# Optimization experiments

Hardware: AMD Instinct MI355X
Metric: run time of the kernel (lower is better)

Reference implementation:

```python
import jax, jax.numpy as jnp
import numpy as np

B, IN_CH, SLOTS, SLOT_SIZE, READ_SLOTS = 16, 512, 10000, 256, 3


def _fa_params(key, c, scale=0.02):
    k1, k2 = jax.random.split(key)
    return (jax.random.normal(k1, (c, c), jnp.float32) * scale, jnp.zeros((c,), jnp.float32),
            jax.random.normal(k2, (c, c), jnp.float32) * scale, jnp.zeros((c,), jnp.float32))


def fast_attention(x, w1, b1, w2, b2):
    # FastAttention: x * Linear2(softmax(Linear1(x), dim=channel))
    h = jax.nn.softmax(x @ w1 + b1, axis=1)
    return x * (h @ w2 + b2)


def setup_inputs() -> dict:
    key = jax.random.key(0)
    ks = jax.random.split(key, 12)
    s = 0.02
    inp = {}
    inp["inputs"] = jax.random.normal(ks[0], (B, IN_CH), jnp.float32)
    inp["memory"] = jax.random.normal(ks[1], (B, SLOTS, SLOT_SIZE), jnp.float32)
    # read_weights branch: FastAttention(IN_CH) -> Linear(IN_CH, READ_SLOTS*SLOTS) -> tanh
    inp["fa_r_w1"], inp["fa_r_b1"], inp["fa_r_w2"], inp["fa_r_b2"] = _fa_params(ks[2], IN_CH)
    inp["W_read"] = jax.random.normal(ks[3], (IN_CH, READ_SLOTS * SLOTS), jnp.float32) * s
    inp["b_read"] = jnp.zeros((READ_SLOTS * SLOTS,), jnp.float32)
    # update_weights branch: FastAttention(IN_CH) -> Linear(IN_CH, READ_SLOTS) -> sigmoid
    inp["fa_u_w1"], inp["fa_u_b1"], inp["fa_u_w2"], inp["fa_u_b2"] = _fa_params(ks[4], IN_CH)
    inp["W_uw"] = jax.random.normal(ks[5], (IN_CH, READ_SLOTS), jnp.float32) * s
    inp["b_uw"] = jnp.zeros((READ_SLOTS,), jnp.float32)
    # update_memory branch: FastAttention(IN_CH+SLOT_SIZE) -> Linear(., SLOT_SIZE) -> relu
    inp["fa_um_w1"], inp["fa_um_b1"], inp["fa_um_w2"], inp["fa_um_b2"] = _fa_params(ks[6], IN_CH + SLOT_SIZE)
    inp["W_um"] = jax.random.normal(ks[7], (IN_CH + SLOT_SIZE, SLOT_SIZE), jnp.float32) * s
    inp["b_um"] = jnp.zeros((SLOT_SIZE,), jnp.float32)
    # apply_memory branch: FastAttention(2*SLOT_SIZE) -> Linear(., SLOT_SIZE) -> relu
    inp["fa_am_w1"], inp["fa_am_b1"], inp["fa_am_w2"], inp["fa_am_b2"] = _fa_params(ks[8], 2 * SLOT_SIZE)
    inp["W_am"] = jax.random.normal(ks[9], (2 * SLOT_SIZE, SLOT_SIZE), jnp.float32) * s
    inp["b_am"] = jnp.zeros((SLOT_SIZE,), jnp.float32)
    return inp


def reference(inputs, memory,
              fa_r_w1, fa_r_b1, fa_r_w2, fa_r_b2, W_read, b_read,
              fa_u_w1, fa_u_b1, fa_u_w2, fa_u_b2, W_uw, b_uw,
              fa_um_w1, fa_um_b1, fa_um_w2, fa_um_b2, W_um, b_um,
              fa_am_w1, fa_am_b1, fa_am_w2, fa_am_b2, W_am, b_am):
    b = inputs.shape[0]
    # read scores: [B, READ_SLOTS, SLOTS]
    read = jnp.tanh(fast_attention(inputs, fa_r_w1, fa_r_b1, fa_r_w2, fa_r_b2) @ W_read + b_read)
    read = read.reshape(b, READ_SLOTS, SLOTS)
    read_w = jnp.max(read, axis=2)                 # [B, READ_SLOTS]
    read_idx = jnp.argmax(read, axis=2)            # [B, READ_SLOTS] int
    upd_w = jax.nn.sigmoid(fast_attention(inputs, fa_u_w1, fa_u_b1, fa_u_w2, fa_u_b2) @ W_uw + b_uw)
    # gather the selected memory slots: [B, READ_SLOTS, SLOT_SIZE]
    r_all = memory[jnp.arange(b)[:, None], read_idx]
    m = jnp.zeros((b, SLOT_SIZE), inputs.dtype)
    # sequential recurrence over the (small, fixed) read_slots
    for i in range(READ_SLOTS):
        r = r_all[:, i]                            # [B, SLOT_SIZE]
        upd = jax.nn.relu(fast_attention(jnp.concatenate([r, inputs], axis=1),
                                         fa_um_w1, fa_um_b1, fa_um_w2, fa_um_b2) @ W_um + b_um)
        u = upd_w[:, i:i + 1]
        r = u * upd + (1.0 - u) * r
        m = read_w[:, i:i + 1] * jax.nn.relu(fast_attention(jnp.concatenate([r, m], axis=1),
                                                            fa_am_w1, fa_am_b1, fa_am_w2, fa_am_b2) @ W_am + b_am)
    return jnp.tanh(m)
```

## Files before the change

### kernel.cpp

```cpp
#include <hip/hip_runtime.h>
#include <cfloat>
#include <cmath>

constexpr int NTILES = 79;

enum : int {
  WS_XR    = 0,
  WS_UPDW  = 8192,
  WS_READW = 8240,
  WS_PMAX  = 8288,
  WS_PIDX  = 12080,
  WS_RNEW  = 15872,
  WS_M     = 28160,
  WS_XC    = 32256,
  WS_TPA   = 69120,
  WS_HA    = 134656,
  WS_YPA   = 151040,
  WS_TPU   = 216576,
  WS_HU    = 437760,
  WS_YPU   = 474624,
  WS_WPU   = 695808,
  WS_TPM   = 769536,
  WS_HM    = 802304,
  WS_YPM   = 810496,
  WS_WPM   = 843264,
};

__device__ __forceinline__ float wave_sum(float v) {
#pragma unroll
  for (int o = 32; o > 0; o >>= 1) v += __shfl_xor(v, o);
  return v;
}
__device__ __forceinline__ float wave_max(float v) {
#pragma unroll
  for (int o = 32; o > 0; o >>= 1) v = fmaxf(v, __shfl_xor(v, o));
  return v;
}
__device__ __forceinline__ float block_sum(float v, float* red) {
  int lane = threadIdx.x & 63, w = threadIdx.x >> 6, nw = blockDim.x >> 6;
  v = wave_sum(v);
  __syncthreads();
  if (lane == 0) red[w] = v;
  __syncthreads();
  float s = 0.f;
  for (int k = 0; k < nw; k++) s += red[k];
  return s;
}
__device__ __forceinline__ float block_max(float v, float* red) {
  int lane = threadIdx.x & 63, w = threadIdx.x >> 6, nw = blockDim.x >> 6;
  v = wave_max(v);
  __syncthreads();
  if (lane == 0) red[w] = v;
  __syncthreads();
  float s = -FLT_MAX;
  for (int k = 0; k < nw; k++) s = fmaxf(s, red[k]);
  return s;
}

__device__ __forceinline__ void mm_tile16(
    const float* __restrict__ xs,
    const float* __restrict__ W, int ldw,
    int koff, int jbase, float2& ra, float2& rb) {
  int lane = threadIdx.x & 63, w = threadIdx.x >> 6;
  const float* xa = xs + (w * 2) * 128;
  const float* xb = xa + 128;
  const float* Wp = W + (size_t)koff * ldw + jbase + lane * 2;
  float a00 = 0.f, a01 = 0.f, a10 = 0.f, a11 = 0.f;
#pragma unroll 8
  for (int k = 0; k < 128; k++) {
    float2 wv = *(const float2*)(Wp + (size_t)k * ldw);
    float xav = xa[k], xbv = xb[k];
    a00 = fmaf(xav, wv.x, a00); a01 = fmaf(xav, wv.y, a01);
    a10 = fmaf(xbv, wv.x, a10); a11 = fmaf(xbv, wv.y, a11);
  }
  ra = make_float2(a00, a01);
  rb = make_float2(a10, a11);
}
__device__ __forceinline__ void store_tile16(
    float* __restrict__ T, int ldt, int jbase, float2 ra, float2 rb) {
  int lane = threadIdx.x & 63, w = threadIdx.x >> 6;
  int r0 = w * 2, j0 = jbase + lane * 2;
  *(float2*)(T + (size_t)r0 * ldt + j0) = ra;
  *(float2*)(T + (size_t)(r0 + 1) * ldt + j0) = rb;
}

__global__ __launch_bounds__(512) void k_mm1_a(
    const float* __restrict__ x, const float* __restrict__ w1r,
    const float* __restrict__ w1u, float* __restrict__ TPA) {
  __shared__ float xs[16 * 128];
  int jt = blockIdx.x, ks = blockIdx.y, m = blockIdx.z, tid = threadIdx.x;
  for (int t = tid; t < 2048; t += 512) {
    int b = t >> 7, kk = t & 127;
    xs[t] = x[b * 512 + ks * 128 + kk];
  }
  __syncthreads();
  float2 ra, rb;
  mm_tile16(xs, m ? w1u : w1r, 512, ks * 128, jt * 128, ra, rb);
  store_tile16(TPA + (size_t)((m * 4 + ks) * 16) * 512, 512, jt * 128, ra, rb);
}

__global__ __launch_bounds__(512) void k_sm_a(
    const float* __restrict__ TPA, const float* __restrict__ b1r,
    const float* __restrict__ b1u, float* __restrict__ HA) {
  __shared__ float red[16];
  int b = blockIdx.x, m = blockIdx.y, tid = threadIdx.x;
  float t = (m ? b1u : b1r)[tid];
#pragma unroll
  for (int ks = 0; ks < 4; ks++)
    t += TPA[(size_t)((m * 4 + ks) * 16 + b) * 512 + tid];
  float mx = block_max(t, red);
  float e = expf(t - mx);
  float s = block_sum(e, red);
  HA[(size_t)(m * 16 + b) * 512 + tid] = e / s;
}

__global__ __launch_bounds__(512) void k_mm2_a(
    const float* __restrict__ HA, const float* __restrict__ w2r,
    const float* __restrict__ w2u, float* __restrict__ YPA) {
  __shared__ float xs[16 * 128];
  int jt = blockIdx.x, ks = blockIdx.y, m = blockIdx.z, tid = threadIdx.x;
  for (int t = tid; t < 2048; t += 512) {
    int b = t >> 7, kk = t & 127;
    xs[t] = HA[(size_t)(m * 16 + b) * 512 + ks * 128 + kk];
  }
  __syncthreads();
  float2 ra, rb;
  mm_tile16(xs, m ? w2u : w2r, 512, ks * 128, jt * 128, ra, rb);
  store_tile16(YPA + (size_t)((m * 4 + ks) * 16) * 512, 512, jt * 128, ra, rb);
}

__global__ __launch_bounds__(512) void k_fin_a(
    const float* __restrict__ x, const float* __restrict__ YPA,
    const float* __restrict__ b2r, const float* __restrict__ b2u,
    const float* __restrict__ Wuw, const float* __restrict__ buw,
    float* __restrict__ XR, float* __restrict__ UPDW, float* __restrict__ M) {
  __shared__ float red[16];
  int b = blockIdx.x, tid = threadIdx.x;
  float yr = b2r[tid], yu = b2u[tid];
#pragma unroll
  for (int ks = 0; ks < 4; ks++) {
    yr += YPA[(size_t)((0 + ks) * 16 + b) * 512 + tid];
    yu += YPA[(size_t)((4 + ks) * 16 + b) * 512 + tid];
  }
  float xv = x[b * 512 + tid];
  XR[b * 512 + tid] = xv * yr;
  float xu = xv * yu;
  if (tid < 256) M[b * 256 + tid] = 0.f;
  for (int i = 0; i < 3; i++) {
    float si = block_sum(xu * Wuw[tid * 3 + i], red);
    if (tid == 0) UPDW[b * 3 + i] = 1.f / (1.f + expf(-(si + buw[i])));
  }
}

__global__ __launch_bounds__(512) void k_read(
    const float* __restrict__ W, const float* __restrict__ brd,
    const float* __restrict__ xr,
    float* __restrict__ pmax, int* __restrict__ pidx) {
  __shared__ __align__(16) float xs[16 * 512];
  int tid = threadIdx.x, lane = tid & 63, w = tid >> 6;
  int i = blockIdx.y, tile = blockIdx.x;
  {
    const float4* s4 = (const float4*)xr;
    float4* d4 = (float4*)xs;
    for (int t = tid; t < 2048; t += 512) d4[t] = s4[t];
  }
  __syncthreads();
  int b0 = w * 2, b1 = b0 + 1;
  int s0 = tile * 128 + lane * 2;
  int sC = (s0 > 9998) ? 9998 : s0;
  const float* Wp = W + i * 10000 + sC;
  const float* xap = xs + b0 * 512;
  const float* xbp = xs + b1 * 512;
  float a00 = 0.f, a01 = 0.f, a10 = 0.f, a11 = 0.f;
#pragma unroll 8
  for (int c = 0; c < 512; c += 4) {
    float4 xa = *(const float4*)(xap + c);
    float4 xb = *(const float4*)(xbp + c);
    float2 w0 = *(const float2*)(Wp + (size_t)(c + 0) * 30000);
    float2 w1 = *(const float2*)(Wp + (size_t)(c + 1) * 30000);
    float2 w2 = *(const float2*)(Wp + (size_t)(c + 2) * 30000);
    float2 w3 = *(const float2*)(Wp + (size_t)(c + 3) * 30000);
    a00 = fmaf(xa.x, w0.x, a00); a01 = fmaf(xa.x, w0.y, a01);
    a10 = fmaf(xb.x, w0.x, a10); a11 = fmaf(xb.x, w0.y, a11);
    a00 = fmaf(xa.y, w1.x, a00); a01 = fmaf(xa.y, w1.y, a01);
    a10 = fmaf(xb.y, w1.x, a10); a11 = fmaf(xb.y, w1.y, a11);
    a00 = fmaf(xa.z, w2.x, a00); a01 = fmaf(xa.z, w2.y, a01);
    a10 = fmaf(xb.z, w2.x, a10); a11 = fmaf(xb.z, w2.y, a11);
    a00 = fmaf(xa.w, w3.x, a00); a01 = fmaf(xa.w, w3.y, a01);
    a10 = fmaf(xb.w, w3.x, a10); a11 = fmaf(xb.w, w3.y, a11);
  }
  float2 bb = *(const float2*)(brd + i * 10000 + sC);
  bool ok0 = (s0 < 10000), ok1 = (s0 + 1 < 10000);
  float v00 = a00 + bb.x, v01 = a01 + bb.y;
  float v10 = a10 + bb.x, v11 = a11 + bb.y;
  float bv0 = ok0 ? v00 : -FLT_MAX; int bi0 = s0;
  if (ok1 && v01 > bv0) { bv0 = v01; bi0 = s0 + 1; }
  float bv1 = ok0 ? v10 : -FLT_MAX; int bi1 = s0;
  if (ok1 && v11 > bv1) { bv1 = v11; bi1 = s0 + 1; }
#pragma unroll
  for (int o = 32; o > 0; o >>= 1) {
    float ov = __shfl_down(bv0, o); int oi = __shfl_down(bi0, o);
    if (ov > bv0) { bv0 = ov; bi0 = oi; }
    ov = __shfl_down(bv1, o); oi = __shfl_down(bi1, o);
    if (ov > bv1) { bv1 = ov; bi1 = oi; }
  }
  if (lane == 0) {
    int base = (i * 16 + b0) * NTILES + tile;
    pmax[base] = bv0; pidx[base] = bi0;
    base = (i * 16 + b1) * NTILES + tile;
    pmax[base] = bv1; pidx[base] = bi1;
  }
}

__global__ __launch_bounds__(768) void k_gather(
    const float* __restrict__ mem, const float* __restrict__ x,
    const float* __restrict__ pmax, const int* __restrict__ pidx,
    float* __restrict__ READW, float* __restrict__ XC) {
  __shared__ int sidx;
  int bi = blockIdx.x, b = bi / 3, i = bi % 3;
  int tid = threadIdx.x, lane = tid & 63;
  if (tid < 64) {
    float bv = -FLT_MAX; int bix = 0;
    const float* pm = pmax + (i * 16 + b) * NTILES;
    const int* pi = pidx + (i * 16 + b) * NTILES;
    for (int t = lane; t < NTILES; t += 64) {
      float v = pm[t]; int ix = pi[t];
      if (v > bv || (v == bv && ix < bix)) { bv = v; bix = ix; }
    }
#pragma unroll
    for (int o = 32; o > 0; o >>= 1) {
      float ov = __shfl_down(bv, o); int oi = __shfl_down(bix, o);
      if (ov > bv || (ov == bv && oi < bix)) { bv = ov; bix = oi; }
    }
    if (lane == 0) { sidx = bix; READW[bi] = tanhf(bv); }
  }
  __syncthreads();
  if (tid < 256) XC[(size_t)bi * 768 + tid] = mem[((size_t)b * 10000 + sidx) * 256 + tid];
  else           XC[(size_t)bi * 768 + tid] = x[b * 512 + (tid - 256)];
}

__global__ __launch_bounds__(512) void k_mm1_u(
    const float* __restrict__ XC, const float* __restrict__ w1um,
    float* __restrict__ TPU) {
  __shared__ float xs[16 * 128];
  int jt = blockIdx.x, ks = blockIdx.y, g = blockIdx.z, tid = threadIdx.x;
  for (int t = tid; t < 2048; t += 512) {
    int r = t >> 7, kk = t & 127;
    xs[t] = XC[(size_t)(g * 16 + r) * 768 + ks * 128 + kk];
  }
  __syncthreads();
  float2 ra, rb;
  mm_tile16(xs, w1um, 768, ks * 128, jt * 128, ra, rb);
  store_tile16(TPU + (size_t)(ks * 48 + g * 16) * 768, 768, jt * 128, ra, rb);
}

__global__ __launch_bounds__(768) void k_sm_u(
    const float* __restrict__ TPU, const float* __restrict__ b1um,
    float* __restrict__ HU) {
  __shared__ float red[16];
  int bi = blockIdx.x, tid = threadIdx.x;
  float t = b1um[tid];
#pragma unroll
  for (int ks = 0; ks < 6; ks++)
    t += TPU[(size_t)(ks * 48 + bi) * 768 + tid];
  float mx = block_max(t, red);
  float e = expf(t - mx);
  float s = block_sum(e, red);
  HU[(size_t)bi * 768 + tid] = e / s;
}

__global__ __launch_bounds__(512) void k_mm2_u(
    const float* __restrict__ HU, const float* __restrict__ w2um,
    float* __restrict__ YPU) {
  __shared__ float xs[16 * 128];
  int jt = blockIdx.x, ks = blockIdx.y, g = blockIdx.z, tid = threadIdx.x;
  for (int t = tid; t < 2048; t += 512) {
    int r = t >> 7, kk = t & 127;
    xs[t] = HU[(size_t)(g * 16 + r) * 768 + ks * 128 + kk];
  }
  __syncthreads();
  float2 ra, rb;
  mm_tile16(xs, w2um, 768, ks * 128, jt * 128, ra, rb);
  store_tile16(YPU + (size_t)(ks * 48 + g * 16) * 768, 768, jt * 128, ra, rb);
}

__global__ __launch_bounds__(512) void k_wum(
    const float* __restrict__ YPU, const float* __restrict__ XC,
    const float* __restrict__ b2um, const float* __restrict__ Wum,
    float* __restrict__ WPU) {
  __shared__ float xs[16 * 128];
  int jt = blockIdx.x, ks = blockIdx.y, g = blockIdx.z, tid = threadIdx.x;
  for (int t = tid; t < 2048; t += 512) {
    int r = t >> 7, kk = t & 127;
    int bi = g * 16 + r, k = ks * 128 + kk;
    float y = b2um[k];
#pragma unroll
    for (int k2 = 0; k2 < 6; k2++) y += YPU[(size_t)(k2 * 48 + bi) * 768 + k];
    xs[t] = XC[(size_t)bi * 768 + k] * y;
  }
  __syncthreads();
  float2 ra, rb;
  mm_tile16(xs, Wum, 256, ks * 128, jt * 128, ra, rb);
  store_tile16(WPU + (size_t)(ks * 48 + g * 16) * 256, 256, jt * 128, ra, rb);
}

__global__ __launch_bounds__(256) void k_fin_u(
    const float* __restrict__ WPU, const float* __restrict__ XC,
    const float* __restrict__ bum, const float* __restrict__ UPDW,
    float* __restrict__ RNEW) {
  int bi = blockIdx.x, tid = threadIdx.x;
  float s = bum[tid];
#pragma unroll
  for (int ks = 0; ks < 6; ks++)
    s += WPU[(size_t)(ks * 48 + bi) * 256 + tid];
  float u = UPDW[bi];
  RNEW[(size_t)bi * 256 + tid] = u * fmaxf(s, 0.f) + (1.f - u) * XC[(size_t)bi * 768 + tid];
}

__global__ __launch_bounds__(512) void k_mm1_m(
    const float* __restrict__ RNEW, const float* __restrict__ M,
    const float* __restrict__ w1am, float* __restrict__ TPM, int i) {
  __shared__ float xs[16 * 128];
  int jt = blockIdx.x, ks = blockIdx.y, tid = threadIdx.x;
  for (int t = tid; t < 2048; t += 512) {
    int b = t >> 7, kk = t & 127;
    xs[t] = (ks < 2) ? RNEW[(size_t)(b * 3 + i) * 256 + ks * 128 + kk]
                     : M[b * 256 + (ks - 2) * 128 + kk];
  }
  __syncthreads();
  float2 ra, rb;
  mm_tile16(xs, w1am, 512, ks * 128, jt * 128, ra, rb);
  store_tile16(TPM + (size_t)(ks * 16) * 512, 512, jt * 128, ra, rb);
}

__global__ __launch_bounds__(512) void k_sm_m(
    const float* __restrict__ TPM, const float* __restrict__ b1am,
    float* __restrict__ HM) {
  __shared__ float red[16];
  int b = blockIdx.x, tid = threadIdx.x;
  float t = b1am[tid];
#pragma unroll
  for (int ks = 0; ks < 4; ks++)
    t += TPM[(size_t)(ks * 16 + b) * 512 + tid];
  float mx = block_max(t, red);
  float e = expf(t - mx);
  float s = block_sum(e, red);
  HM[(size_t)b * 512 + tid] = e / s;
}

__global__ __launch_bounds__(512) void k_mm2_m(
    const float* __restrict__ HM, const float* __restrict__ w2am,
    float* __restrict__ YPM) {
  __shared__ float xs[16 * 128];
  int jt = blockIdx.x, ks = blockIdx.y, tid = threadIdx.x;
  for (int t = tid; t < 2048; t += 512) {
    int b = t >> 7, kk = t & 127;
    xs[t] = HM[(size_t)b * 512 + ks * 128 + kk];
  }
  __syncthreads();
  float2 ra, rb;
  mm_tile16(xs, w2am, 512, ks * 128, jt * 128, ra, rb);
  store_tile16(YPM + (size_t)(ks * 16) * 512, 512, jt * 128, ra, rb);
}

__global__ __launch_bounds__(512) void k_wam(
    const float* __restrict__ YPM, const float* __restrict__ RNEW,
    const float* __restrict__ M, const float* __restrict__ b2am,
    const float* __restrict__ Wam, float* __restrict__ WPM, int i) {
  __shared__ float xs[16 * 128];
  int jt = blockIdx.x, ks = blockIdx.y, tid = threadIdx.x;
  for (int t = tid; t < 2048; t += 512) {
    int b = t >> 7, kk = t & 127;
    int k = ks * 128 + kk;
    float xc = (ks < 2) ? RNEW[(size_t)(b * 3 + i) * 256 + k]
                        : M[b * 256 + k - 256];
    float y = b2am[k];
#pragma unroll
    for (int k2 = 0; k2 < 4; k2++) y += YPM[(size_t)(k2 * 16 + b) * 512 + k];
    xs[t] = xc * y;
  }
  __syncthreads();
  float2 ra, rb;
  mm_tile16(xs, Wam, 256, ks * 128, jt * 128, ra, rb);
  store_tile16(WPM + (size_t)(ks * 16) * 256, 256, jt * 128, ra, rb);
}

__global__ __launch_bounds__(256) void k_fin_m(
    const float* __restrict__ WPM, const float* __restrict__ bam,
    const float* __restrict__ READW, float* __restrict__ M,
    float* __restrict__ out, int i, int last) {
  int b = blockIdx.x, tid = threadIdx.x;
  float s = bam[tid];
#pragma unroll
  for (int ks = 0; ks < 4; ks++)
    s += WPM[(size_t)(ks * 16 + b) * 256 + tid];
  float mv = READW[b * 3 + i] * fmaxf(s, 0.f);
  M[b * 256 + tid] = mv;
  if (last) out[b * 256 + tid] = tanhf(mv);
}

extern "C" void kernel_launch(void* const* d_in, const int* in_sizes, int n_in,
                              void* d_out, int out_size, void* d_ws, size_t ws_size,
                              hipStream_t stream) {
  const float* x    = (const float*)d_in[0];
  const float* mem  = (const float*)d_in[1];
  const float* w1r  = (const float*)d_in[2];
  const float* b1r  = (const float*)d_in[3];
  const float* w2r  = (const float*)d_in[4];
  const float* b2r  = (const float*)d_in[5];
  const float* Wrd  = (const float*)d_in[6];
  const float* brd  = (const float*)d_in[7];
  const float* w1u  = (const float*)d_in[8];
  const float* b1u  = (const float*)d_in[9];
  const float* w2u  = (const float*)d_in[10];
  const float* b2u  = (const float*)d_in[11];
  const float* Wuw  = (const float*)d_in[12];
  const float* buw  = (const float*)d_in[13];
  const float* w1um = (const float*)d_in[14];
  const float* b1um = (const float*)d_in[15];
  const float* w2um = (const float*)d_in[16];
  const float* b2um = (const float*)d_in[17];
  const float* Wum  = (const float*)d_in[18];
  const float* bum  = (const float*)d_in[19];
  const float* w1am = (const float*)d_in[20];
  const float* b1am = (const float*)d_in[21];
  const float* w2am = (const float*)d_in[22];
  const float* b2am = (const float*)d_in[23];
  const float* Wam  = (const float*)d_in[24];
  const float* bam  = (const float*)d_in[25];

  float* ws   = (float*)d_ws;
  float* XR   = ws + WS_XR;
  float* UPDW = ws + WS_UPDW;
  float* RDW  = ws + WS_READW;
  float* PMAX = ws + WS_PMAX;
  int*   PIDX = (int*)(ws + WS_PIDX);
  float* RNEW = ws + WS_RNEW;
  float* M    = ws + WS_M;
  float* XC   = ws + WS_XC;
  float* TPA  = ws + WS_TPA;
  float* HA   = ws + WS_HA;
  float* YPA  = ws + WS_YPA;
  float* TPU  = ws + WS_TPU;
  float* HU   = ws + WS_HU;
  float* YPU  = ws + WS_YPU;
  float* WPU  = ws + WS_WPU;
  float* TPM  = ws + WS_TPM;
  float* HM   = ws + WS_HM;
  float* YPM  = ws + WS_YPM;
  float* WPM  = ws + WS_WPM;
  float* out  = (float*)d_out;

  k_mm1_a<<<dim3(4, 4, 2), 512, 0, stream>>>(x, w1r, w1u, TPA);
  k_sm_a <<<dim3(16, 2),   512, 0, stream>>>(TPA, b1r, b1u, HA);
  k_mm2_a<<<dim3(4, 4, 2), 512, 0, stream>>>(HA, w2r, w2u, YPA);
  k_fin_a<<<16,            512, 0, stream>>>(x, YPA, b2r, b2u, Wuw, buw,
                                             XR, UPDW, M);
  k_read  <<<dim3(NTILES, 3), 512, 0, stream>>>(Wrd, brd, XR, PMAX, PIDX);
  k_gather<<<48,              768, 0, stream>>>(mem, x, PMAX, PIDX, RDW, XC);
  k_mm1_u<<<dim3(6, 6, 3), 512, 0, stream>>>(XC, w1um, TPU);
  k_sm_u <<<48,            768, 0, stream>>>(TPU, b1um, HU);
  k_mm2_u<<<dim3(6, 6, 3), 512, 0, stream>>>(HU, w2um, YPU);
  k_wum  <<<dim3(2, 6, 3), 512, 0, stream>>>(YPU, XC, b2um, Wum, WPU);
  k_fin_u<<<48,            256, 0, stream>>>(WPU, XC, bum, UPDW, RNEW);
  for (int i = 0; i < 3; i++) {
    k_mm1_m<<<dim3(4, 4), 512, 0, stream>>>(RNEW, M, w1am, TPM, i);
    k_sm_m <<<16,         512, 0, stream>>>(TPM, b1am, HM);
    k_mm2_m<<<dim3(4, 4), 512, 0, stream>>>(HM, w2am, YPM);
    k_wam  <<<dim3(2, 4), 512, 0, stream>>>(YPM, RNEW, M, b2am, Wam, WPM, i);
    k_fin_m<<<16,         256, 0, stream>>>(WPM, bam, RDW, M, out, i, i == 2);
  }
}
```

Measured before the change: 508.1 us.

## Fuse all stages into one cooperative persistent kernel with grid barriers

Replaces the chain of about 26 small kernel launches with a single cooperative kernel of 256 blocks that steps through the stages, separated by atomic grid-wide barriers. It also fuses softmax with the second FastAttention matmul and the x-multiply, so the HA/YPA/HU/YPU intermediate buffers go away. The aim is to remove per-launch overhead and the tiny-grid tail latency that dominate this latency-bound chain. In exchange, stages with few blocks leave most CUs idle, each block now does more serial work (the full K=512/768 reduction), and every barrier costs a global atomic spin.

```diff
diff --git a/kernel.cpp b/kernel.cpp
--- a/kernel.cpp
+++ b/kernel.cpp
@@ -14,16 +14,23 @@
   WS_M     = 28160,
   WS_XC    = 32256,
   WS_TPA   = 69120,
-  WS_HA    = 134656,
-  WS_YPA   = 151040,
+  WS_BAR   = 134656,
+  WS_XU    = 151040,
   WS_TPU   = 216576,
-  WS_HU    = 437760,
-  WS_YPU   = 474624,
-  WS_WPU   = 695808,
+  WS_XU2   = 474624,
   WS_TPM   = 769536,
-  WS_HM    = 802304,
-  WS_YPM   = 810496,
-  WS_WPM   = 843264,
+  WS_XA    = 810496,
+};
+
+struct Params {
+  const float *x, *mem;
+  const float *w1r, *b1r, *w2r, *b2r, *Wrd, *brd;
+  const float *w1u, *b1u, *w2u, *b2u, *Wuw, *buw;
+  const float *w1um, *b1um, *w2um, *b2um, *Wum, *bum;
+  const float *w1am, *b1am, *w2am, *b2am, *Wam, *bam;
+  float *XR, *XU, *UPDW, *RDW, *PMAX;
+  int   *PIDX;
+  float *RNEW, *M, *XC, *TPA, *TPU, *XU2, *TPM, *XA, *out;
 };
 
 __device__ __forceinline__ float wave_sum(float v) {
@@ -46,28 +53,28 @@
   for (int k = 0; k < nw; k++) s += red[k];
   return s;
 }
-__device__ __forceinline__ float block_max(float v, float* red) {
-  int lane = threadIdx.x & 63, w = threadIdx.x >> 6, nw = blockDim.x >> 6;
-  v = wave_max(v);
+
+__device__ __forceinline__ void grid_sync(unsigned* bar, unsigned target) {
   __syncthreads();
-  if (lane == 0) red[w] = v;
+  if (threadIdx.x == 0) {
+    __threadfence();
+    __hip_atomic_fetch_add(bar, 1u, __ATOMIC_RELEASE, __HIP_MEMORY_SCOPE_AGENT);
+    while (__hip_atomic_load(bar, __ATOMIC_ACQUIRE, __HIP_MEMORY_SCOPE_AGENT) < target)
+      __builtin_amdgcn_s_sleep(2);
+  }
   __syncthreads();
-  float s = -FLT_MAX;
-  for (int k = 0; k < nw; k++) s = fmaxf(s, red[k]);
-  return s;
-}
-
-__device__ __forceinline__ void mm_tile16(
-    const float* __restrict__ xs,
-    const float* __restrict__ W, int ldw,
-    int koff, int jbase, float2& ra, float2& rb) {
+}
+
+__device__ __forceinline__ void mm_rows(const float* __restrict__ xs, int ldx, int K,
+                                        const float* __restrict__ W, int ldw, int jbase,
+                                        float2& ra, float2& rb) {
   int lane = threadIdx.x & 63, w = threadIdx.x >> 6;
-  const float* xa = xs + (w * 2) * 128;
-  const float* xb = xa + 128;
-  const float* Wp = W + (size_t)koff * ldw + jbase + lane * 2;
+  const float* xa = xs + (w * 2) * ldx;
+  const float* xb = xa + ldx;
+  const float* Wp = W + jbase + lane * 2;
   float a00 = 0.f, a01 = 0.f, a10 = 0.f, a11 = 0.f;
 #pragma unroll 8
-  for (int k = 0; k < 128; k++) {
+  for (int k = 0; k < K; k++) {
     float2 wv = *(const float2*)(Wp + (size_t)k * ldw);
     float xav = xa[k], xbv = xb[k];
     a00 = fmaf(xav, wv.x, a00); a01 = fmaf(xav, wv.y, a01);
@@ -76,398 +83,347 @@
   ra = make_float2(a00, a01);
   rb = make_float2(a10, a11);
 }
-__device__ __forceinline__ void store_tile16(
-    float* __restrict__ T, int ldt, int jbase, float2 ra, float2 rb) {
+__device__ __forceinline__ void store_tile16(float* __restrict__ T, int ldt, int jbase,
+                                             float2 ra, float2 rb) {
   int lane = threadIdx.x & 63, w = threadIdx.x >> 6;
   int r0 = w * 2, j0 = jbase + lane * 2;
   *(float2*)(T + (size_t)r0 * ldt + j0) = ra;
   *(float2*)(T + (size_t)(r0 + 1) * ldt + j0) = rb;
 }
 
-__global__ __launch_bounds__(512) void k_mm1_a(
-    const float* __restrict__ x, const float* __restrict__ w1r,
-    const float* __restrict__ w1u, float* __restrict__ TPA) {
-  __shared__ float xs[16 * 128];
-  int jt = blockIdx.x, ks = blockIdx.y, m = blockIdx.z, tid = threadIdx.x;
-  for (int t = tid; t < 2048; t += 512) {
-    int b = t >> 7, kk = t & 127;
-    xs[t] = x[b * 512 + ks * 128 + kk];
-  }
-  __syncthreads();
-  float2 ra, rb;
-  mm_tile16(xs, m ? w1u : w1r, 512, ks * 128, jt * 128, ra, rb);
-  store_tile16(TPA + (size_t)((m * 4 + ks) * 16) * 512, 512, jt * 128, ra, rb);
-}
-
-__global__ __launch_bounds__(512) void k_sm_a(
-    const float* __restrict__ TPA, const float* __restrict__ b1r,
-    const float* __restrict__ b1u, float* __restrict__ HA) {
+__device__ __forceinline__ void softmax_rows(float* xs, int ncol) {
+  int lane = threadIdx.x & 63, w = threadIdx.x >> 6;
+#pragma unroll
+  for (int rr = 0; rr < 2; rr++) {
+    float* row = xs + (size_t)(w * 2 + rr) * ncol;
+    float mx = -FLT_MAX;
+    for (int j = lane; j < ncol; j += 64) mx = fmaxf(mx, row[j]);
+    mx = wave_max(mx);
+    float acc = 0.f;
+    for (int j = lane; j < ncol; j += 64) {
+      float e = expf(row[j] - mx);
+      row[j] = e;
+      acc += e;
+    }
+    acc = wave_sum(acc);
+    float inv = 1.f / acc;
+    for (int j = lane; j < ncol; j += 64) row[j] *= inv;
+  }
+}
+
+__global__ __launch_bounds__(512, 2) void mega(Params p, unsigned* bar) {
+  __shared__ __align__(16) float xs[12288];
   __shared__ float red[16];
-  int b = blockIdx.x, m = blockIdx.y, tid = threadIdx.x;
-  float t = (m ? b1u : b1r)[tid];
-#pragma unroll
-  for (int ks = 0; ks < 4; ks++)
-    t += TPA[(size_t)((m * 4 + ks) * 16 + b) * 512 + tid];
-  float mx = block_max(t, red);
-  float e = expf(t - mx);
-  float s = block_sum(e, red);
-  HA[(size_t)(m * 16 + b) * 512 + tid] = e / s;
-}
-
-__global__ __launch_bounds__(512) void k_mm2_a(
-    const float* __restrict__ HA, const float* __restrict__ w2r,
-    const float* __restrict__ w2u, float* __restrict__ YPA) {
-  __shared__ float xs[16 * 128];
-  int jt = blockIdx.x, ks = blockIdx.y, m = blockIdx.z, tid = threadIdx.x;
-  for (int t = tid; t < 2048; t += 512) {
-    int b = t >> 7, kk = t & 127;
-    xs[t] = HA[(size_t)(m * 16 + b) * 512 + ks * 128 + kk];
-  }
-  __syncthreads();
-  float2 ra, rb;
-  mm_tile16(xs, m ? w2u : w2r, 512, ks * 128, jt * 128, ra, rb);
-  store_tile16(YPA + (size_t)((m * 4 + ks) * 16) * 512, 512, jt * 128, ra, rb);
-}
-
-__global__ __launch_bounds__(512) void k_fin_a(
-    const float* __restrict__ x, const float* __restrict__ YPA,
-    const float* __restrict__ b2r, const float* __restrict__ b2u,
-    const float* __restrict__ Wuw, const float* __restrict__ buw,
-    float* __restrict__ XR, float* __restrict__ UPDW, float* __restrict__ M) {
-  __shared__ float red[16];
-  int b = blockIdx.x, tid = threadIdx.x;
-  float yr = b2r[tid], yu = b2u[tid];
-#pragma unroll
-  for (int ks = 0; ks < 4; ks++) {
-    yr += YPA[(size_t)((0 + ks) * 16 + b) * 512 + tid];
-    yu += YPA[(size_t)((4 + ks) * 16 + b) * 512 + tid];
-  }
-  float xv = x[b * 512 + tid];
-  XR[b * 512 + tid] = xv * yr;
-  float xu = xv * yu;
-  if (tid < 256) M[b * 256 + tid] = 0.f;
+  __shared__ int sidx;
+  const int bid = blockIdx.x, tid = threadIdx.x;
+  const int lane = tid & 63, w = tid >> 6;
+  unsigned ph = 0;
+#define GSYNC() do { ++ph; grid_sync(bar, ph * 256u); } while (0)
+
+  if (bid < 32) {
+    int jt = bid & 3, ks = (bid >> 2) & 3, m = bid >> 4;
+    for (int t = tid; t < 2048; t += 512) {
+      int b = t >> 7, kk = t & 127;
+      xs[t] = p.x[b * 512 + ks * 128 + kk];
+    }
+    __syncthreads();
+    float2 ra, rb;
+    mm_rows(xs, 128, 128, (m ? p.w1u : p.w1r) + (size_t)(ks * 128) * 512, 512, jt * 128, ra, rb);
+    store_tile16(p.TPA + (size_t)((m * 4 + ks) * 16) * 512, 512, jt * 128, ra, rb);
+  }
+  GSYNC();
+
+  if (bid < 8) {
+    int m = bid >> 2, jt = bid & 3;
+    const float* b1 = m ? p.b1u : p.b1r;
+    for (int e = tid; e < 8192; e += 512) {
+      int b = e >> 9, j = e & 511;
+      float v = b1[j];
+#pragma unroll
+      for (int ks = 0; ks < 4; ks++) v += p.TPA[(size_t)((m * 4 + ks) * 16 + b) * 512 + j];
+      xs[e] = v;
+    }
+    __syncthreads();
+    softmax_rows(xs, 512);
+    float2 ra, rb;
+    mm_rows(xs, 512, 512, m ? p.w2u : p.w2r, 512, jt * 128, ra, rb);
+    int r0 = w * 2, j0 = jt * 128 + lane * 2;
+    const float* b2 = m ? p.b2u : p.b2r;
+    float b20 = b2[j0], b21 = b2[j0 + 1];
+    float* dst = m ? p.XU : p.XR;
+    float2 x0 = *(const float2*)(p.x + r0 * 512 + j0);
+    float2 x1 = *(const float2*)(p.x + (r0 + 1) * 512 + j0);
+    *(float2*)(dst + r0 * 512 + j0)       = make_float2(x0.x * (ra.x + b20), x0.y * (ra.y + b21));
+    *(float2*)(dst + (r0 + 1) * 512 + j0) = make_float2(x1.x * (rb.x + b20), x1.y * (rb.y + b21));
+  }
+  GSYNC();
+
+  if (bid < 237) {
+    int ii = bid / NTILES, tile = bid % NTILES;
+    {
+      const float4* s4 = (const float4*)p.XR;
+      float4* d4 = (float4*)xs;
+      for (int t = tid; t < 2048; t += 512) d4[t] = s4[t];
+    }
+    __syncthreads();
+    int b0 = w * 2, b1 = b0 + 1;
+    int s0 = tile * 128 + lane * 2;
+    int sC = (s0 > 9998) ? 9998 : s0;
+    const float* Wp = p.Wrd + ii * 10000 + sC;
+    const float* xap = xs + b0 * 512;
+    const float* xbp = xs + b1 * 512;
+    float a00 = 0.f, a01 = 0.f, a10 = 0.f, a11 = 0.f;
+#pragma unroll 8
+    for (int c = 0; c < 512; c += 4) {
+      float4 xa = *(const float4*)(xap + c);
+      float4 xb = *(const float4*)(xbp + c);
+      float2 w0 = *(const float2*)(Wp + (size_t)(c + 0) * 30000);
+      float2 w1 = *(const float2*)(Wp + (size_t)(c + 1) * 30000);
+      float2 w2 = *(const float2*)(Wp + (size_t)(c + 2) * 30000);
+      float2 w3 = *(const float2*)(Wp + (size_t)(c + 3) * 30000);
+      a00 = fmaf(xa.x, w0.x, a00); a01 = fmaf(xa.x, w0.y, a01);
+      a10 = fmaf(xb.x, w0.x, a10); a11 = fmaf(xb.x, w0.y, a11);
+      a00 = fmaf(xa.y, w1.x, a00); a01 = fmaf(xa.y, w1.y, a01);
+      a10 = fmaf(xb.y, w1.x, a10); a11 = fmaf(xb.y, w1.y, a11);
+      a00 = fmaf(xa.z, w2.x, a00); a01 = fmaf(xa.z, w2.y, a01);
+      a10 = fmaf(xb.z, w2.x, a10); a11 = fmaf(xb.z, w2.y, a11);
+      a00 = fmaf(xa.w, w3.x, a00); a01 = fmaf(xa.w, w3.y, a01);
+      a10 = fmaf(xb.w, w3.x, a10); a11 = fmaf(xb.w, w3.y, a11);
+    }
+    float2 bb = *(const float2*)(p.brd + ii * 10000 + sC);
+    bool ok0 = (s0 < 10000), ok1 = (s0 + 1 < 10000);
+    float v00 = a00 + bb.x, v01 = a01 + bb.y;
+    float v10 = a10 + bb.x, v11 = a11 + bb.y;
+    float bv0 = ok0 ? v00 : -FLT_MAX; int bi0 = s0;
+    if (ok1 && v01 > bv0) { bv0 = v01; bi0 = s0 + 1; }
+    float bv1 = ok0 ? v10 : -FLT_MAX; int bi1 = s0;
+    if (ok1 && v11 > bv1) { bv1 = v11; bi1 = s0 + 1; }
+#pragma unroll
+    for (int o = 32; o > 0; o >>= 1) {
+      float ov = __shfl_down(bv0, o); int oi = __shfl_down(bi0, o);
+      if (ov > bv0) { bv0 = ov; bi0 = oi; }
+      ov = __shfl_down(bv1, o); oi = __shfl_down(bi1, o);
+      if (ov > bv1) { bv1 = ov; bi1 = oi; }
+    }
+    if (lane == 0) {
+      int base = (ii * 16 + b0) * NTILES + tile;
+      p.PMAX[base] = bv0; p.PIDX[base] = bi0;
+      base = (ii * 16 + b1) * NTILES + tile;
+      p.PMAX[base] = bv1; p.PIDX[base] = bi1;
+    }
+  } else if (bid >= 240) {
+    int b = bid - 240;
+    float xu = p.XU[b * 512 + tid];
+    if (tid < 256) p.M[b * 256 + tid] = 0.f;
+    for (int i2 = 0; i2 < 3; i2++) {
+      float si = block_sum(xu * p.Wuw[tid * 3 + i2], red);
+      if (tid == 0) p.UPDW[b * 3 + i2] = 1.f / (1.f + expf(-(si + p.buw[i2])));
+    }
+  }
+  GSYNC();
+
+  if (bid < 48) {
+    int b = bid / 3, ii = bid % 3;
+    if (tid < 64) {
+      float bv = -FLT_MAX; int bix = 0;
+      const float* pm = p.PMAX + (ii * 16 + b) * NTILES;
+      const int* pi = p.PIDX + (ii * 16 + b) * NTILES;
+      for (int t = tid; t < NTILES; t += 64) {
+        float v = pm[t]; int ix = pi[t];
+        if (v > bv || (v == bv && ix < bix)) { bv = v; bix = ix; }
+      }
+#pragma unroll
+      for (int o = 32; o > 0; o >>= 1) {
+        float ov = __shfl_down(bv, o); int oi = __shfl_down(bix, o);
+        if (ov > bv || (ov == bv && oi < bix)) { bv = ov; bix = oi; }
+      }
+      if (tid == 0) { sidx = bix; p.RDW[bid] = tanhf(bv); }
+    }
+    __syncthreads();
+    for (int t = tid; t < 768; t += 512)
+      p.XC[(size_t)bid * 768 + t] = (t < 256)
+          ? p.mem[((size_t)b * 10000 + sidx) * 256 + t]
+          : p.x[b * 512 + (t - 256)];
+  }
+  GSYNC();
+
+  if (bid < 108) {
+    int jt = bid % 6, ks = (bid / 6) % 6, g = bid / 36;
+    for (int t = tid; t < 2048; t += 512) {
+      int r = t >> 7, kk = t & 127;
+      xs[t] = p.XC[(size_t)(g * 16 + r) * 768 + ks * 128 + kk];
+    }
+    __syncthreads();
+    float2 ra, rb;
+    mm_rows(xs, 128, 128, p.w1um + (size_t)(ks * 128) * 768, 768, jt * 128, ra, rb);
+    store_tile16(p.TPU + (size_t)(ks * 48 + g * 16) * 768, 768, jt * 128, ra, rb);
+  }
+  GSYNC();
+
+  if (bid < 18) {
+    int g = bid / 6, jt = bid % 6;
+    for (int e = tid; e < 12288; e += 512) {
+      int r = e / 768, j = e - r * 768;
+      float v = p.b1um[j];
+#pragma unroll
+      for (int ks = 0; ks < 6; ks++) v += p.TPU[(size_t)(ks * 48 + g * 16 + r) * 768 + j];
+      xs[e] = v;
+    }
+    __syncthreads();
+    softmax_rows(xs, 768);
+    float2 ra, rb;
+    mm_rows(xs, 768, 768, p.w2um, 768, jt * 128, ra, rb);
+    int r0 = w * 2, j0 = jt * 128 + lane * 2, bi0 = g * 16 + r0;
+    float b0 = p.b2um[j0], b1v = p.b2um[j0 + 1];
+    float2 xc0 = *(const float2*)(p.XC + (size_t)bi0 * 768 + j0);
+    float2 xc1 = *(const float2*)(p.XC + (size_t)(bi0 + 1) * 768 + j0);
+    *(float2*)(p.XU2 + (size_t)bi0 * 768 + j0) =
+        make_float2(xc0.x * (ra.x + b0), xc0.y * (ra.y + b1v));
+    *(float2*)(p.XU2 + (size_t)(bi0 + 1) * 768 + j0) =
+        make_float2(xc1.x * (rb.x + b0), xc1.y * (rb.y + b1v));
+  }
+  GSYNC();
+
+  if (bid < 6) {
+    int g = bid >> 1, jt = bid & 1;
+    const float* src = p.XU2 + (size_t)(g * 16) * 768;
+    for (int e = tid; e < 12288; e += 512) xs[e] = src[e];
+    __syncthreads();
+    float2 ra, rb;
+    mm_rows(xs, 768, 768, p.Wum, 256, jt * 128, ra, rb);
+    int r0 = w * 2, j0 = jt * 128 + lane * 2, bi0 = g * 16 + r0;
+    float bb0 = p.bum[j0], bb1 = p.bum[j0 + 1];
+    float u0 = p.UPDW[bi0], u1 = p.UPDW[bi0 + 1];
+    float2 xc0 = *(const float2*)(p.XC + (size_t)bi0 * 768 + j0);
+    float2 xc1 = *(const float2*)(p.XC + (size_t)(bi0 + 1) * 768 + j0);
+    *(float2*)(p.RNEW + (size_t)bi0 * 256 + j0) =
+        make_float2(u0 * fmaxf(ra.x + bb0, 0.f) + (1.f - u0) * xc0.x,
+                    u0 * fmaxf(ra.y + bb1, 0.f) + (1.f - u0) * xc0.y);
+    *(float2*)(p.RNEW + (size_t)(bi0 + 1) * 256 + j0) =
+        make_float2(u1 * fmaxf(rb.x + bb0, 0.f) + (1.f - u1) * xc1.x,
+                    u1 * fmaxf(rb.y + bb1, 0.f) + (1.f - u1) * xc1.y);
+  }
+  GSYNC();
+
   for (int i = 0; i < 3; i++) {
-    float si = block_sum(xu * Wuw[tid * 3 + i], red);
-    if (tid == 0) UPDW[b * 3 + i] = 1.f / (1.f + expf(-(si + buw[i])));
-  }
-}
-
-__global__ __launch_bounds__(512) void k_read(
-    const float* __restrict__ W, const float* __restrict__ brd,
-    const float* __restrict__ xr,
-    float* __restrict__ pmax, int* __restrict__ pidx) {
-  __shared__ __align__(16) float xs[16 * 512];
-  int tid = threadIdx.x, lane = tid & 63, w = tid >> 6;
-  int i = blockIdx.y, tile = blockIdx.x;
-  {
-    const float4* s4 = (const float4*)xr;
-    float4* d4 = (float4*)xs;
-    for (int t = tid; t < 2048; t += 512) d4[t] = s4[t];
-  }
-  __syncthreads();
-  int b0 = w * 2, b1 = b0 + 1;
-  int s0 = tile * 128 + lane * 2;
-  int sC = (s0 > 9998) ? 9998 : s0;
-  const float* Wp = W + i * 10000 + sC;
-  const float* xap = xs + b0 * 512;
-  const float* xbp = xs + b1 * 512;
-  float a00 = 0.f, a01 = 0.f, a10 = 0.f, a11 = 0.f;
-#pragma unroll 8
-  for (int c = 0; c < 512; c += 4) {
-    float4 xa = *(const float4*)(xap + c);
-    float4 xb = *(const float4*)(xbp + c);
-    float2 w0 = *(const float2*)(Wp + (size_t)(c + 0) * 30000);
-    float2 w1 = *(const float2*)(Wp + (size_t)(c + 1) * 30000);
-    float2 w2 = *(const float2*)(Wp + (size_t)(c + 2) * 30000);
-    float2 w3 = *(const float2*)(Wp + (size_t)(c + 3) * 30000);
-    a00 = fmaf(xa.x, w0.x, a00); a01 = fmaf(xa.x, w0.y, a01);
-    a10 = fmaf(xb.x, w0.x, a10); a11 = fmaf(xb.x, w0.y, a11);
-    a00 = fmaf(xa.y, w1.x, a00); a01 = fmaf(xa.y, w1.y, a01);
-    a10 = fmaf(xb.y, w1.x, a10); a11 = fmaf(xb.y, w1.y, a11);
-    a00 = fmaf(xa.z, w2.x, a00); a01 = fmaf(xa.z, w2.y, a01);
-    a10 = fmaf(xb.z, w2.x, a10); a11 = fmaf(xb.z, w2.y, a11);
-    a00 = fmaf(xa.w, w3.x, a00); a01 = fmaf(xa.w, w3.y, a01);
-    a10 = fmaf(xb.w, w3.x, a10); a11 = fmaf(xb.w, w3.y, a11);
-  }
-  float2 bb = *(const float2*)(brd + i * 10000 + sC);
-  bool ok0 = (s0 < 10000), ok1 = (s0 + 1 < 10000);
-  float v00 = a00 + bb.x, v01 = a01 + bb.y;
-  float v10 = a10 + bb.x, v11 = a11 + bb.y;
-  float bv0 = ok0 ? v00 : -FLT_MAX; int bi0 = s0;
-  if (ok1 && v01 > bv0) { bv0 = v01; bi0 = s0 + 1; }
-  float bv1 = ok0 ? v10 : -FLT_MAX; int bi1 = s0;
-  if (ok1 && v11 > bv1) { bv1 = v11; bi1 = s0 + 1; }
-#pragma unroll
-  for (int o = 32; o > 0; o >>= 1) {
-    float ov = __shfl_down(bv0, o); int oi = __shfl_down(bi0, o);
-    if (ov > bv0) { bv0 = ov; bi0 = oi; }
-    ov = __shfl_down(bv1, o); oi = __shfl_down(bi1, o);
-    if (ov > bv1) { bv1 = ov; bi1 = oi; }
-  }
-  if (lane == 0) {
-    int base = (i * 16 + b0) * NTILES + tile;
-    pmax[base] = bv0; pidx[base] = bi0;
-    base = (i * 16 + b1) * NTILES + tile;
-    pmax[base] = bv1; pidx[base] = bi1;
-  }
-}
-
-__global__ __launch_bounds__(768) void k_gather(
-    const float* __restrict__ mem, const float* __restrict__ x,
-    const float* __restrict__ pmax, const int* __restrict__ pidx,
-    float* __restrict__ READW, float* __restrict__ XC) {
-  __shared__ int sidx;
-  int bi = blockIdx.x, b = bi / 3, i = bi % 3;
-  int tid = threadIdx.x, lane = tid & 63;
-  if (tid < 64) {
-    float bv = -FLT_MAX; int bix = 0;
-    const float* pm = pmax + (i * 16 + b) * NTILES;
-    const int* pi = pidx + (i * 16 + b) * NTILES;
-    for (int t = lane; t < NTILES; t += 64) {
-      float v = pm[t]; int ix = pi[t];
-      if (v > bv || (v == bv && ix < bix)) { bv = v; bix = ix; }
-    }
-#pragma unroll
-    for (int o = 32; o > 0; o >>= 1) {
-      float ov = __shfl_down(bv, o); int oi = __shfl_down(bix, o);
-      if (ov > bv || (ov == bv && oi < bix)) { bv = ov; bix = oi; }
-    }
-    if (lane == 0) { sidx = bix; READW[bi] = tanhf(bv); }
-  }
-  __syncthreads();
-  if (tid < 256) XC[(size_t)bi * 768 + tid] = mem[((size_t)b * 10000 + sidx) * 256 + tid];
-  else           XC[(size_t)bi * 768 + tid] = x[b * 512 + (tid - 256)];
-}
-
-__global__ __launch_bounds__(512) void k_mm1_u(
-    const float* __restrict__ XC, const float* __restrict__ w1um,
-    float* __restrict__ TPU) {
-  __shared__ float xs[16 * 128];
-  int jt = blockIdx.x, ks = blockIdx.y, g = blockIdx.z, tid = threadIdx.x;
-  for (int t = tid; t < 2048; t += 512) {
-    int r = t >> 7, kk = t & 127;
-    xs[t] = XC[(size_t)(g * 16 + r) * 768 + ks * 128 + kk];
-  }
-  __syncthreads();
-  float2 ra, rb;
-  mm_tile16(xs, w1um, 768, ks * 128, jt * 128, ra, rb);
-  store_tile16(TPU + (size_t)(ks * 48 + g * 16) * 768, 768, jt * 128, ra, rb);
-}
-
-__global__ __launch_bounds__(768) void k_sm_u(
-    const float* __restrict__ TPU, const float* __restrict__ b1um,
-    float* __restrict__ HU) {
-  __shared__ float red[16];
-  int bi = blockIdx.x, tid = threadIdx.x;
-  float t = b1um[tid];
-#pragma unroll
-  for (int ks = 0; ks < 6; ks++)
-    t += TPU[(size_t)(ks * 48 + bi) * 768 + tid];
-  float mx = block_max(t, red);
-  float e = expf(t - mx);
-  float s = block_sum(e, red);
-  HU[(size_t)bi * 768 + tid] = e / s;
-}
-
-__global__ __launch_bounds__(512) void k_mm2_u(
-    const float* __restrict__ HU, const float* __restrict__ w2um,
-    float* __restrict__ YPU) {
-  __shared__ float xs[16 * 128];
-  int jt = blockIdx.x, ks = blockIdx.y, g = blockIdx.z, tid = threadIdx.x;
-  for (int t = tid; t < 2048; t += 512) {
-    int r = t >> 7, kk = t & 127;
-    xs[t] = HU[(size_t)(g * 16 + r) * 768 + ks * 128 + kk];
-  }
-  __syncthreads();
-  float2 ra, rb;
-  mm_tile16(xs, w2um, 768, ks * 128, jt * 128, ra, rb);
-  store_tile16(YPU + (size_t)(ks * 48 + g * 16) * 768, 768, jt * 128, ra, rb);
-}
-
-__global__ __launch_bounds__(512) void k_wum(
-    const float* __restrict__ YPU, const float* __restrict__ XC,
-    const float* __restrict__ b2um, const float* __restrict__ Wum,
-    float* __restrict__ WPU) {
-  __shared__ float xs[16 * 128];
-  int jt = blockIdx.x, ks = blockIdx.y, g = blockIdx.z, tid = threadIdx.x;
-  for (int t = tid; t < 2048; t += 512) {
-    int r = t >> 7, kk = t & 127;
-    int bi = g * 16 + r, k = ks * 128 + kk;
-    float y = b2um[k];
-#pragma unroll
-    for (int k2 = 0; k2 < 6; k2++) y += YPU[(size_t)(k2 * 48 + bi) * 768 + k];
-    xs[t] = XC[(size_t)bi * 768 + k] * y;
-  }
-  __syncthreads();
-  float2 ra, rb;
-  mm_tile16(xs, Wum, 256, ks * 128, jt * 128, ra, rb);
-  store_tile16(WPU + (size_t)(ks * 48 + g * 16) * 256, 256, jt * 128, ra, rb);
-}
-
-__global__ __launch_bounds__(256) void k_fin_u(
-    const float* __restrict__ WPU, const float* __restrict__ XC,
-    const float* __restrict__ bum, const float* __restrict__ UPDW,
-    float* __restrict__ RNEW) {
-  int bi = blockIdx.x, tid = threadIdx.x;
-  float s = bum[tid];
-#pragma unroll
-  for (int ks = 0; ks < 6; ks++)
-    s += WPU[(size_t)(ks * 48 + bi) * 256 + tid];
-  float u = UPDW[bi];
-  RNEW[(size_t)bi * 256 + tid] = u * fmaxf(s, 0.f) + (1.f - u) * XC[(size_t)bi * 768 + tid];
-}
-
-__global__ __launch_bounds__(512) void k_mm1_m(
-    const float* __restrict__ RNEW, const float* __restrict__ M,
-    const float* __restrict__ w1am, float* __restrict__ TPM, int i) {
-  __shared__ float xs[16 * 128];
-  int jt = blockIdx.x, ks = blockIdx.y, tid = threadIdx.x;
-  for (int t = tid; t < 2048; t += 512) {
-    int b = t >> 7, kk = t & 127;
-    xs[t] = (ks < 2) ? RNEW[(size_t)(b * 3 + i) * 256 + ks * 128 + kk]
-                     : M[b * 256 + (ks - 2) * 128 + kk];
-  }
-  __syncthreads();
-  float2 ra, rb;
-  mm_tile16(xs, w1am, 512, ks * 128, jt * 128, ra, rb);
-  store_tile16(TPM + (size_t)(ks * 16) * 512, 512, jt * 128, ra, rb);
-}
-
-__global__ __launch_bounds__(512) void k_sm_m(
-    const float* __restrict__ TPM, const float* __restrict__ b1am,
-    float* __restrict__ HM) {
-  __shared__ float red[16];
-  int b = blockIdx.x, tid = threadIdx.x;
-  float t = b1am[tid];
-#pragma unroll
-  for (int ks = 0; ks < 4; ks++)
-    t += TPM[(size_t)(ks * 16 + b) * 512 + tid];
-  float mx = block_max(t, red);
-  float e = expf(t - mx);
-  float s = block_sum(e, red);
-  HM[(size_t)b * 512 + tid] = e / s;
-}
-
-__global__ __launch_bounds__(512) void k_mm2_m(
-    const float* __restrict__ HM, const float* __restrict__ w2am,
-    float* __restrict__ YPM) {
-  __shared__ float xs[16 * 128];
-  int jt = blockIdx.x, ks = blockIdx.y, tid = threadIdx.x;
-  for (int t = tid; t < 2048; t += 512) {
-    int b = t >> 7, kk = t & 127;
-    xs[t] = HM[(size_t)b * 512 + ks * 128 + kk];
-  }
-  __syncthreads();
-  float2 ra, rb;
-  mm_tile16(xs, w2am, 512, ks * 128, jt * 128, ra, rb);
-  store_tile16(YPM + (size_t)(ks * 16) * 512, 512, jt * 128, ra, rb);
-}
-
-__global__ __launch_bounds__(512) void k_wam(
-    const float* __restrict__ YPM, const float* __restrict__ RNEW,
-    const float* __restrict__ M, const float* __restrict__ b2am,
-    const float* __restrict__ Wam, float* __restrict__ WPM, int i) {
-  __shared__ float xs[16 * 128];
-  int jt = blockIdx.x, ks = blockIdx.y, tid = threadIdx.x;
-  for (int t = tid; t < 2048; t += 512) {
-    int b = t >> 7, kk = t & 127;
-    int k = ks * 128 + kk;
-    float xc = (ks < 2) ? RNEW[(size_t)(b * 3 + i) * 256 + k]
-                        : M[b * 256 + k - 256];
-    float y = b2am[k];
-#pragma unroll
-    for (int k2 = 0; k2 < 4; k2++) y += YPM[(size_t)(k2 * 16 + b) * 512 + k];
-    xs[t] = xc * y;
-  }
-  __syncthreads();
-  float2 ra, rb;
-  mm_tile16(xs, Wam, 256, ks * 128, jt * 128, ra, rb);
-  store_tile16(WPM + (size_t)(ks * 16) * 256, 256, jt * 128, ra, rb);
-}
-
-__global__ __launch_bounds__(256) void k_fin_m(
-    const float* __restrict__ WPM, const float* __restrict__ bam,
-    const float* __restrict__ READW, float* __restrict__ M,
-    float* __restrict__ out, int i, int last) {
-  int b = blockIdx.x, tid = threadIdx.x;
-  float s = bam[tid];
-#pragma unroll
-  for (int ks = 0; ks < 4; ks++)
-    s += WPM[(size_t)(ks * 16 + b) * 256 + tid];
-  float mv = READW[b * 3 + i] * fmaxf(s, 0.f);
-  M[b * 256 + tid] = mv;
-  if (last) out[b * 256 + tid] = tanhf(mv);
+    if (bid < 16) {
+      int jt = bid & 3, ks = bid >> 2;
+      for (int t = tid; t < 2048; t += 512) {
+        int b = t >> 7, kk = t & 127;
+        xs[t] = (ks < 2) ? p.RNEW[(size_t)(b * 3 + i) * 256 + ks * 128 + kk]
+                         : p.M[b * 256 + (ks - 2) * 128 + kk];
+      }
+      __syncthreads();
+      float2 ra, rb;
+      mm_rows(xs, 128, 128, p.w1am + (size_t)(ks * 128) * 512, 512, jt * 128, ra, rb);
+      store_tile16(p.TPM + (size_t)(ks * 16) * 512, 512, jt * 128, ra, rb);
+    }
+    GSYNC();
+    if (bid < 4) {
+      int jt = bid;
+      for (int e = tid; e < 8192; e += 512) {
+        int b = e >> 9, j = e & 511;
+        float v = p.b1am[j];
+#pragma unroll
+        for (int ks = 0; ks < 4; ks++) v += p.TPM[(size_t)(ks * 16 + b) * 512 + j];
+        xs[e] = v;
+      }
+      __syncthreads();
+      softmax_rows(xs, 512);
+      float2 ra, rb;
+      mm_rows(xs, 512, 512, p.w2am, 512, jt * 128, ra, rb);
+      int r0 = w * 2, j0 = jt * 128 + lane * 2;
+      float b0 = p.b2am[j0], b1v = p.b2am[j0 + 1];
+      float2 c0, c1;
+      if (j0 < 256) {
+        c0 = *(const float2*)(p.RNEW + (size_t)(r0 * 3 + i) * 256 + j0);
+        c1 = *(const float2*)(p.RNEW + (size_t)((r0 + 1) * 3 + i) * 256 + j0);
+      } else {
+        c0 = *(const float2*)(p.M + r0 * 256 + (j0 - 256));
+        c1 = *(const float2*)(p.M + (r0 + 1) * 256 + (j0 - 256));
+      }
+      *(float2*)(p.XA + r0 * 512 + j0) =
+          make_float2(c0.x * (ra.x + b0), c0.y * (ra.y + b1v));
+      *(float2*)(p.XA + (r0 + 1) * 512 + j0) =
+          make_float2(c1.x * (rb.x + b0), c1.y * (rb.y + b1v));
+    }
+    GSYNC();
+    if (bid < 2) {
+      int jt = bid;
+      for (int e = tid; e < 8192; e += 512) xs[e] = p.XA[e];
+      __syncthreads();
+      float2 ra, rb;
+      mm_rows(xs, 512, 512, p.Wam, 256, jt * 128, ra, rb);
+      int r0 = w * 2, j0 = jt * 128 + lane * 2;
+      float bb0 = p.bam[j0], bb1 = p.bam[j0 + 1];
+      float u0 = p.RDW[r0 * 3 + i], u1 = p.RDW[(r0 + 1) * 3 + i];
+      float m00 = u0 * fmaxf(ra.x + bb0, 0.f), m01 = u0 * fmaxf(ra.y + bb1, 0.f);
+      float m10 = u1 * fmaxf(rb.x + bb0, 0.f), m11 = u1 * fmaxf(rb.y + bb1, 0.f);
+      *(float2*)(p.M + r0 * 256 + j0) = make_float2(m00, m01);
+      *(float2*)(p.M + (r0 + 1) * 256 + j0) = make_float2(m10, m11);
+      if (i == 2) {
+        *(float2*)(p.out + r0 * 256 + j0) = make_float2(tanhf(m00), tanhf(m01));
+        *(float2*)(p.out + (r0 + 1) * 256 + j0) = make_float2(tanhf(m10), tanhf(m11));
+      }
+    }
+    if (i < 2) GSYNC();
+  }
+#undef GSYNC
+}
+
+__global__ void k_init(unsigned* bar) {
+  if (threadIdx.x == 0) *bar = 0u;
 }
 
 extern "C" void kernel_launch(void* const* d_in, const int* in_sizes, int n_in,
                               void* d_out, int out_size, void* d_ws, size_t ws_size,
                               hipStream_t stream) {
-  const float* x    = (const float*)d_in[0];
-  const float* mem  = (const float*)d_in[1];
-  const float* w1r  = (const float*)d_in[2];
-  const float* b1r  = (const float*)d_in[3];
-  const float* w2r  = (const float*)d_in[4];
-  const float* b2r  = (const float*)d_in[5];
-  const float* Wrd  = (const float*)d_in[6];
-  const float* brd  = (const float*)d_in[7];
-  const float* w1u  = (const float*)d_in[8];
-  const float* b1u  = (const float*)d_in[9];
-  const float* w2u  = (const float*)d_in[10];
-  const float* b2u  = (const float*)d_in[11];
-  const float* Wuw  = (const float*)d_in[12];
-  const float* buw  = (const float*)d_in[13];
-  const float* w1um = (const float*)d_in[14];
-  const float* b1um = (const float*)d_in[15];
-  const float* w2um = (const float*)d_in[16];
-  const float* b2um = (const float*)d_in[17];
-  const float* Wum  = (const float*)d_in[18];
-  const float* bum  = (const float*)d_in[19];
-  const float* w1am = (const float*)d_in[20];
-  const float* b1am = (const float*)d_in[21];
-  const float* w2am = (const float*)d_in[22];
-  const float* b2am = (const float*)d_in[23];
-  const float* Wam  = (const float*)d_in[24];
-  const float* bam  = (const float*)d_in[25];
-
-  float* ws   = (float*)d_ws;
-  float* XR   = ws + WS_XR;
-  float* UPDW = ws + WS_UPDW;
-  float* RDW  = ws + WS_READW;
-  float* PMAX = ws + WS_PMAX;
-  int*   PIDX = (int*)(ws + WS_PIDX);
-  float* RNEW = ws + WS_RNEW;
-  float* M    = ws + WS_M;
-  float* XC   = ws + WS_XC;
-  float* TPA  = ws + WS_TPA;
-  float* HA   = ws + WS_HA;
-  float* YPA  = ws + WS_YPA;
-  float* TPU  = ws + WS_TPU;
-  float* HU   = ws + WS_HU;
-  float* YPU  = ws + WS_YPU;
-  float* WPU  = ws + WS_WPU;
-  float* TPM  = ws + WS_TPM;
-  float* HM   = ws + WS_HM;
-  float* YPM  = ws + WS_YPM;
-  float* WPM  = ws + WS_WPM;
-  float* out  = (float*)d_out;
-
-  k_mm1_a<<<dim3(4, 4, 2), 512, 0, stream>>>(x, w1r, w1u, TPA);
-  k_sm_a <<<dim3(16, 2),   512, 0, stream>>>(TPA, b1r, b1u, HA);
-  k_mm2_a<<<dim3(4, 4, 2), 512, 0, stream>>>(HA, w2r, w2u, YPA);
-  k_fin_a<<<16,            512, 0, stream>>>(x, YPA, b2r, b2u, Wuw, buw,
-                                             XR, UPDW, M);
-  k_read  <<<dim3(NTILES, 3), 512, 0, stream>>>(Wrd, brd, XR, PMAX, PIDX);
-  k_gather<<<48,              768, 0, stream>>>(mem, x, PMAX, PIDX, RDW, XC);
-  k_mm1_u<<<dim3(6, 6, 3), 512, 0, stream>>>(XC, w1um, TPU);
-  k_sm_u <<<48,            768, 0, stream>>>(TPU, b1um, HU);
-  k_mm2_u<<<dim3(6, 6, 3), 512, 0, stream>>>(HU, w2um, YPU);
-  k_wum  <<<dim3(2, 6, 3), 512, 0, stream>>>(YPU, XC, b2um, Wum, WPU);
-  k_fin_u<<<48,            256, 0, stream>>>(WPU, XC, bum, UPDW, RNEW);
-  for (int i = 0; i < 3; i++) {
-    k_mm1_m<<<dim3(4, 4), 512, 0, stream>>>(RNEW, M, w1am, TPM, i);
-    k_sm_m <<<16,         512, 0, stream>>>(TPM, b1am, HM);
-    k_mm2_m<<<dim3(4, 4), 512, 0, stream>>>(HM, w2am, YPM);
-    k_wam  <<<dim3(2, 4), 512, 0, stream>>>(YPM, RNEW, M, b2am, Wam, WPM, i);
-    k_fin_m<<<16,         256, 0, stream>>>(WPM, bam, RDW, M, out, i, i == 2);
-  }
-}
+  float* ws = (float*)d_ws;
+  Params p;
+  p.x    = (const float*)d_in[0];
+  p.mem  = (const float*)d_in[1];
+  p.w1r  = (const float*)d_in[2];
+  p.b1r  = (const float*)d_in[3];
+  p.w2r  = (const float*)d_in[4];
+  p.b2r  = (const float*)d_in[5];
+  p.Wrd  = (const float*)d_in[6];
+  p.brd  = (const float*)d_in[7];
+  p.w1u  = (const float*)d_in[8];
+  p.b1u  = (const float*)d_in[9];
+  p.w2u  = (const float*)d_in[10];
+  p.b2u  = (const float*)d_in[11];
+  p.Wuw  = (const float*)d_in[12];
+  p.buw  = (const float*)d_in[13];
+  p.w1um = (const float*)d_in[14];
+  p.b1um = (const float*)d_in[15];
+  p.w2um = (const float*)d_in[16];
+  p.b2um = (const float*)d_in[17];
+  p.Wum  = (const float*)d_in[18];
+  p.bum  = (const float*)d_in[19];
+  p.w1am = (const float*)d_in[20];
+  p.b1am = (const float*)d_in[21];
+  p.w2am = (const float*)d_in[22];
+  p.b2am = (const float*)d_in[23];
+  p.Wam  = (const float*)d_in[24];
+  p.bam  = (const float*)d_in[25];
+  p.XR   = ws + WS_XR;
+  p.XU   = ws + WS_XU;
+  p.UPDW = ws + WS_UPDW;
+  p.RDW  = ws + WS_READW;
+  p.PMAX = ws + WS_PMAX;
+  p.PIDX = (int*)(ws + WS_PIDX);
+  p.RNEW = ws + WS_RNEW;
+  p.M    = ws + WS_M;
+  p.XC   = ws + WS_XC;
+  p.TPA  = ws + WS_TPA;
+  p.TPU  = ws + WS_TPU;
+  p.XU2  = ws + WS_XU2;
+  p.TPM  = ws + WS_TPM;
+  p.XA   = ws + WS_XA;
+  p.out  = (float*)d_out;
+  unsigned* bar = (unsigned*)(ws + WS_BAR);
+
+  hipLaunchKernelGGL(k_init, dim3(1), dim3(64), 0, stream, bar);
+  void* kargs[] = { (void*)&p, (void*)&bar };
+  hipLaunchCooperativeKernel((void*)mega, dim3(256), dim3(512), kargs, 0, stream);
+}
```

New measurement: 1.870 ms. 3.68x slower.
